# Performance work log

Hardware: AMD Instinct MI355X
Metric: run time of the kernel (lower is better)

Reference implementation:

```python
import jax, jax.numpy as jnp
import numpy as np

STRIPE = 8
EPS = 1e-5  # PyTorch BatchNorm default eps


def setup_inputs() -> dict:
    key = jax.random.key(0)
    ks = jax.random.split(key, 8)
    b, c, t, h, w = 4, 256, 8, 128, 64
    ic = c // 2  # inter_channels default = in_channels // 2
    scale = 0.02
    return {
        "x": jax.random.normal(ks[0], (b, c, t, h, w), jnp.float32),
        # 1x1 Conv3d weights are just channel-mixing matrices (out, in)
        "g_w": jax.random.normal(ks[1], (ic, c), jnp.float32) * scale,
        "g_b": jnp.zeros((ic,), jnp.float32),
        "theta_w": jax.random.normal(ks[2], (ic, c), jnp.float32) * scale,
        "theta_b": jnp.zeros((ic,), jnp.float32),
        "phi_w": jax.random.normal(ks[3], (ic, c), jnp.float32) * scale,
        "phi_b": jnp.zeros((ic,), jnp.float32),
        "W_w": jax.random.normal(ks[4], (c, ic), jnp.float32) * scale,
        "W_b": jnp.zeros((c,), jnp.float32),
        # BatchNorm3d (eval mode): original inits gamma=beta=0; use nonzero
        # gamma here so the reference output is non-trivial.
        "bn_gamma": jax.random.normal(ks[5], (c,), jnp.float32) * 0.1,
        "bn_beta": jax.random.normal(ks[6], (c,), jnp.float32) * 0.1,
        "bn_mean": jnp.zeros((c,), jnp.float32),
        "bn_var": jnp.ones((c,), jnp.float32),
    }


def reference(x, g_w, g_b, theta_w, theta_b, phi_w, phi_b,
              W_w, W_b, bn_gamma, bn_beta, bn_mean, bn_var):
    b, c, t, h, w = x.shape
    hs = h // STRIPE
    # stripe mean-pool: AdaptiveAvgPool2d(1) over each (hs, w) stripe region
    xr = x.reshape(b, c, t, STRIPE, hs, w)
    d = xr.mean(axis=(4, 5))                      # (b, c, t, stripe)
    S = t * STRIPE
    dn = d.reshape(b, c, S)                       # tokens: (b, c, S)
    # 1x1 conv3d projections == channel matmuls
    g = jnp.einsum('bcs,ic->bsi', dn, g_w) + g_b          # (b, S, ic)
    th = jnp.einsum('bcs,ic->bsi', dn, theta_w) + theta_b  # (b, S, ic)
    ph = jnp.einsum('bcs,ic->bsi', dn, phi_w) + phi_b      # (b, S, ic)
    # small self-attention over stripe tokens
    f = jnp.einsum('bsi,bri->bsr', th, ph)                 # (b, S, S)
    attn = jax.nn.softmax(f, axis=-1)                      # instance='soft'
    y = jnp.einsum('bsr,bri->bsi', attn, g)                # (b, S, ic)
    # output 1x1 conv + BatchNorm3d (eval mode, running stats)
    Wy = jnp.einsum('bsi,ci->bcs', y, W_w) + W_b[None, :, None]  # (b, c, S)
    inv = bn_gamma / jnp.sqrt(bn_var + EPS)
    Wy = (Wy - bn_mean[None, :, None]) * inv[None, :, None] + bn_beta[None, :, None]
    # broadcast each stripe value back over its (hs, w) region + residual
    Wy = Wy.reshape(b, c, t, STRIPE, 1, 1)
    z = (xr + Wy).reshape(b, c, t, h, w)
    return z
```

## Files before the change

### kernel.cpp

```cpp
#include <hip/hip_runtime.h>
#include <hip/hip_bf16.h>
#include <math.h>

#define B 4
#define C 256
#define T 8
#define H 128
#define WW 64
#define IC 128
#define S 64
#define NSTRIPE 8
#define HS 16
#define REGION 1024
#define EPS 1e-5f

__global__ void pool_kernel(const float* __restrict__ x, float* __restrict__ dn) {
    int sb = blockIdx.x;
    const float4* xr = (const float4*)(x + (size_t)sb * REGION);
    float4 v = xr[threadIdx.x];
    float sum = v.x + v.y + v.z + v.w;
    #pragma unroll
    for (int off = 32; off > 0; off >>= 1)
        sum += __shfl_down(sum, off, 64);
    __shared__ float ws[4];
    int wid = threadIdx.x >> 6;
    int lane = threadIdx.x & 63;
    if (lane == 0) ws[wid] = sum;
    __syncthreads();
    if (threadIdx.x == 0) {
        float tot = ws[0] + ws[1] + ws[2] + ws[3];
        dn[sb] = tot * (1.0f / (float)REGION);
    }
}

__global__ void proj_kernel(const float* __restrict__ dn,
                            const float* __restrict__ gw, const float* __restrict__ gb,
                            const float* __restrict__ tw, const float* __restrict__ tb,
                            const float* __restrict__ pw, const float* __restrict__ pb,
                            float* __restrict__ g, float* __restrict__ th,
                            float* __restrict__ ph) {
    int blk = blockIdx.x;
    int b = blk >> 6, s = blk & 63;
    __shared__ float dloc[C];
    for (int ch = threadIdx.x; ch < C; ch += blockDim.x)
        dloc[ch] = dn[(b * C + ch) * S + s];
    __syncthreads();
    int i = threadIdx.x;
    float ag = gb[i], at = tb[i], ap = pb[i];
    const float* gwr = gw + i * C;
    const float* twr = tw + i * C;
    const float* pwr = pw + i * C;
    for (int ch = 0; ch < C; ++ch) {
        float d = dloc[ch];
        ag = fmaf(d, gwr[ch], ag);
        at = fmaf(d, twr[ch], at);
        ap = fmaf(d, pwr[ch], ap);
    }
    size_t o = ((size_t)(b * S + s)) * IC + i;
    g[o] = ag; th[o] = at; ph[o] = ap;
}

__global__ void attn_kernel(const float* __restrict__ g,
                            const float* __restrict__ th,
                            const float* __restrict__ ph,
                            float* __restrict__ y) {
    int blk = blockIdx.x;
    int b = blk >> 6, s = blk & 63;
    __shared__ float p[S];
    __shared__ float thloc[IC];
    int tid = threadIdx.x;
    thloc[tid] = th[((size_t)(b * S + s)) * IC + tid];
    __syncthreads();
    if (tid < 64) {
        int r = tid;
        const float* phr = ph + ((size_t)(b * S + r)) * IC;
        float f = 0.0f;
        for (int i = 0; i < IC; ++i) f = fmaf(thloc[i], phr[i], f);
        float m = f;
        #pragma unroll
        for (int off = 32; off > 0; off >>= 1)
            m = fmaxf(m, __shfl_xor(m, off, 64));
        float e = __expf(f - m);
        float sum = e;
        #pragma unroll
        for (int off = 32; off > 0; off >>= 1)
            sum += __shfl_xor(sum, off, 64);
        p[r] = e / sum;
    }
    __syncthreads();
    int i = tid;
    float acc = 0.0f;
    for (int r = 0; r < S; ++r)
        acc = fmaf(p[r], g[((size_t)(b * S + r)) * IC + i], acc);
    y[((size_t)(b * S + s)) * IC + i] = acc;
}

__global__ void outproj_kernel(const float* __restrict__ y,
                               const float* __restrict__ Ww, const float* __restrict__ Wb,
                               const float* __restrict__ gamma, const float* __restrict__ beta,
                               const float* __restrict__ mean, const float* __restrict__ var,
                               float* __restrict__ wy) {
    int idx = blockIdx.x * blockDim.x + threadIdx.x;
    int s = idx & 63;
    int ch = (idx >> 6) & 255;
    int b = idx >> 14;
    const float* yr = y + ((size_t)(b * S + s)) * IC;
    const float* wr = Ww + (size_t)ch * IC;
    float acc = Wb[ch];
    for (int i = 0; i < IC; ++i) acc = fmaf(yr[i], wr[i], acc);
    float inv = gamma[ch] * rsqrtf(var[ch] + EPS);
    wy[idx] = (acc - mean[ch]) * inv + beta[ch];
}

__global__ void add_kernel(const float* __restrict__ x,
                           const float* __restrict__ wy,
                           float* __restrict__ out) {
    size_t f = (size_t)blockIdx.x * blockDim.x + threadIdx.x;
    const float4* x4 = (const float4*)x;
    float4* o4 = (float4*)out;
    float4 v = x4[f];
    float a = wy[f >> 8];
    v.x += a; v.y += a; v.z += a; v.w += a;
    o4[f] = v;
}

extern "C" void kernel_launch(void* const* d_in, const int* in_sizes, int n_in,
                              void* d_out, int out_size, void* d_ws, size_t ws_size,
                              hipStream_t stream) {
    const float* x       = (const float*)d_in[0];
    const float* g_w     = (const float*)d_in[1];
    const float* g_b     = (const float*)d_in[2];
    const float* theta_w = (const float*)d_in[3];
    const float* theta_b = (const float*)d_in[4];
    const float* phi_w   = (const float*)d_in[5];
    const float* phi_b   = (const float*)d_in[6];
    const float* W_w     = (const float*)d_in[7];
    const float* W_b     = (const float*)d_in[8];
    const float* bn_g    = (const float*)d_in[9];
    const float* bn_b    = (const float*)d_in[10];
    const float* bn_m    = (const float*)d_in[11];
    const float* bn_v    = (const float*)d_in[12];
    float* out = (float*)d_out;

    float* ws = (float*)d_ws;
    float* dn = ws;
    float* g  = dn + B * C * S;
    float* th = g  + B * S * IC;
    float* ph = th + B * S * IC;
    float* y  = ph + B * S * IC;
    float* wy = y  + B * S * IC;

    const int nRegions = B * C * T * NSTRIPE;
    pool_kernel<<<nRegions, 256, 0, stream>>>(x, dn);

    proj_kernel<<<B * S, IC, 0, stream>>>(dn, g_w, g_b, theta_w, theta_b,
                                          phi_w, phi_b, g, th, ph);

    attn_kernel<<<B * S, IC, 0, stream>>>(g, th, ph, y);

    outproj_kernel<<<(B * C * S) / 256, 256, 0, stream>>>(y, W_w, W_b,
                                                          bn_g, bn_b, bn_m, bn_v, wy);

    const size_t nVec4 = (size_t)B * C * T * H * WW / 4;
    add_kernel<<<(int)(nVec4 / 256), 256, 0, stream>>>(x, wy, out);
}
```

Baseline: 514.8 us.

## Fuse attention with output projection and retile pooling and projection kernels

Pooling now has one wavefront per region and writes the token-major layout (b,s,c), so the projection kernel can load its input with contiguous float4 reads. The projection kernel runs the three projections on 384 threads, one weight matrix per group of 128, using vectorized weight reads. Attention, the output 1x1 conv and BatchNorm are fused into one kernel that stages g in shared memory, which removes the y buffer and one launch. The add kernel reads the wy buffer with the new transposed indexing. The total time is still dominated by the memory-bound pool and add passes over x.

```diff
diff --git a/kernel.cpp b/kernel.cpp
--- a/kernel.cpp
+++ b/kernel.cpp
@@ -1,5 +1,4 @@
 #include <hip/hip_runtime.h>
-#include <hip/hip_bf16.h>
 #include <math.h>
 
 #define B 4
@@ -15,21 +14,24 @@
 #define EPS 1e-5f
 
 __global__ void pool_kernel(const float* __restrict__ x, float* __restrict__ dn) {
-    int sb = blockIdx.x;
+    int wid = threadIdx.x >> 6;
+    int lane = threadIdx.x & 63;
+    int sb = blockIdx.x * 4 + wid;
     const float4* xr = (const float4*)(x + (size_t)sb * REGION);
-    float4 v = xr[threadIdx.x];
-    float sum = v.x + v.y + v.z + v.w;
+    float sum = 0.0f;
+    #pragma unroll
+    for (int k = 0; k < 4; ++k) {
+        float4 v = xr[k * 64 + lane];
+        sum += v.x + v.y + v.z + v.w;
+    }
     #pragma unroll
     for (int off = 32; off > 0; off >>= 1)
         sum += __shfl_down(sum, off, 64);
-    __shared__ float ws[4];
-    int wid = threadIdx.x >> 6;
-    int lane = threadIdx.x & 63;
-    if (lane == 0) ws[wid] = sum;
-    __syncthreads();
-    if (threadIdx.x == 0) {
-        float tot = ws[0] + ws[1] + ws[2] + ws[3];
-        dn[sb] = tot * (1.0f / (float)REGION);
+    if (lane == 0) {
+        int b = sb >> 14;
+        int c = (sb >> 6) & 255;
+        int s = sb & 63;
+        dn[(((size_t)b << 6) | s) * C + c] = sum * (1.0f / (float)REGION);
     }
 }
 
@@ -40,76 +42,124 @@
                             float* __restrict__ g, float* __restrict__ th,
                             float* __restrict__ ph) {
     int blk = blockIdx.x;
-    int b = blk >> 6, s = blk & 63;
-    __shared__ float dloc[C];
-    for (int ch = threadIdx.x; ch < C; ch += blockDim.x)
-        dloc[ch] = dn[(b * C + ch) * S + s];
-    __syncthreads();
-    int i = threadIdx.x;
-    float ag = gb[i], at = tb[i], ap = pb[i];
-    const float* gwr = gw + i * C;
-    const float* twr = tw + i * C;
-    const float* pwr = pw + i * C;
-    for (int ch = 0; ch < C; ++ch) {
-        float d = dloc[ch];
-        ag = fmaf(d, gwr[ch], ag);
-        at = fmaf(d, twr[ch], at);
-        ap = fmaf(d, pwr[ch], ap);
-    }
-    size_t o = ((size_t)(b * S + s)) * IC + i;
-    g[o] = ag; th[o] = at; ph[o] = ap;
-}
-
-__global__ void attn_kernel(const float* __restrict__ g,
-                            const float* __restrict__ th,
-                            const float* __restrict__ ph,
-                            float* __restrict__ y) {
+    __shared__ float4 dloc[C / 4];
+    int tid = threadIdx.x;
+    if (tid < C / 4)
+        dloc[tid] = ((const float4*)(dn + (size_t)blk * C))[tid];
+    __syncthreads();
+    int p = tid >> 7;
+    int i = tid & 127;
+    const float* wsel = (p == 0) ? gw : (p == 1) ? tw : pw;
+    const float* bsel = (p == 0) ? gb : (p == 1) ? tb : pb;
+    float* osel      = (p == 0) ? g  : (p == 1) ? th : ph;
+    const float4* wr = (const float4*)(wsel + (size_t)i * C);
+    float4 a = {0.f, 0.f, 0.f, 0.f};
+    #pragma unroll 8
+    for (int k = 0; k < C / 4; ++k) {
+        float4 wv = wr[k];
+        float4 dv = dloc[k];
+        a.x = fmaf(dv.x, wv.x, a.x);
+        a.y = fmaf(dv.y, wv.y, a.y);
+        a.z = fmaf(dv.z, wv.z, a.z);
+        a.w = fmaf(dv.w, wv.w, a.w);
+    }
+    osel[(size_t)blk * IC + i] = a.x + a.y + a.z + a.w + bsel[i];
+}
+
+__global__ void attn_out_kernel(const float* __restrict__ g,
+                                const float* __restrict__ th,
+                                const float* __restrict__ ph,
+                                const float* __restrict__ Ww, const float* __restrict__ Wb,
+                                const float* __restrict__ gamma, const float* __restrict__ beta,
+                                const float* __restrict__ mean, const float* __restrict__ var,
+                                float* __restrict__ wy) {
     int blk = blockIdx.x;
-    int b = blk >> 6, s = blk & 63;
-    __shared__ float p[S];
+    int b = blk >> 6;
+    int tid = threadIdx.x;
+
     __shared__ float thloc[IC];
-    int tid = threadIdx.x;
-    thloc[tid] = th[((size_t)(b * S + s)) * IC + tid];
-    __syncthreads();
+    __shared__ float gloc[S][IC];
+    __shared__ float sc[S];
+    __shared__ float pvals[S];
+    __shared__ float ypart[2][IC];
+    __shared__ float yloc[IC];
+
+    if (tid < IC) thloc[tid] = th[(size_t)blk * IC + tid];
+    {
+        const float4* gsrc = (const float4*)(g + (size_t)(b * S) * IC);
+        float4* gdst = (float4*)&gloc[0][0];
+        #pragma unroll
+        for (int k = 0; k < (S * IC / 4) / 256; ++k)
+            gdst[k * 256 + tid] = gsrc[k * 256 + tid];
+    }
+    __syncthreads();
+
+    {
+        int r = tid >> 2, q = tid & 3;
+        const float4* phr = (const float4*)(ph + (size_t)(b * S + r) * IC) + q * 8;
+        const float4* th4 = (const float4*)thloc + q * 8;
+        float4 a = {0.f, 0.f, 0.f, 0.f};
+        #pragma unroll
+        for (int k = 0; k < 8; ++k) {
+            float4 pv = phr[k];
+            float4 tv = th4[k];
+            a.x = fmaf(tv.x, pv.x, a.x);
+            a.y = fmaf(tv.y, pv.y, a.y);
+            a.z = fmaf(tv.z, pv.z, a.z);
+            a.w = fmaf(tv.w, pv.w, a.w);
+        }
+        float f = a.x + a.y + a.z + a.w;
+        f += __shfl_xor(f, 1, 64);
+        f += __shfl_xor(f, 2, 64);
+        if (q == 0) sc[r] = f;
+    }
+    __syncthreads();
+
     if (tid < 64) {
-        int r = tid;
-        const float* phr = ph + ((size_t)(b * S + r)) * IC;
-        float f = 0.0f;
-        for (int i = 0; i < IC; ++i) f = fmaf(thloc[i], phr[i], f);
-        float m = f;
+        float v = sc[tid];
+        float m = v;
         #pragma unroll
         for (int off = 32; off > 0; off >>= 1)
             m = fmaxf(m, __shfl_xor(m, off, 64));
-        float e = __expf(f - m);
+        float e = __expf(v - m);
         float sum = e;
         #pragma unroll
         for (int off = 32; off > 0; off >>= 1)
             sum += __shfl_xor(sum, off, 64);
-        p[r] = e / sum;
-    }
-    __syncthreads();
-    int i = tid;
-    float acc = 0.0f;
-    for (int r = 0; r < S; ++r)
-        acc = fmaf(p[r], g[((size_t)(b * S + r)) * IC + i], acc);
-    y[((size_t)(b * S + s)) * IC + i] = acc;
-}
-
-__global__ void outproj_kernel(const float* __restrict__ y,
-                               const float* __restrict__ Ww, const float* __restrict__ Wb,
-                               const float* __restrict__ gamma, const float* __restrict__ beta,
-                               const float* __restrict__ mean, const float* __restrict__ var,
-                               float* __restrict__ wy) {
-    int idx = blockIdx.x * blockDim.x + threadIdx.x;
-    int s = idx & 63;
-    int ch = (idx >> 6) & 255;
-    int b = idx >> 14;
-    const float* yr = y + ((size_t)(b * S + s)) * IC;
-    const float* wr = Ww + (size_t)ch * IC;
-    float acc = Wb[ch];
-    for (int i = 0; i < IC; ++i) acc = fmaf(yr[i], wr[i], acc);
-    float inv = gamma[ch] * rsqrtf(var[ch] + EPS);
-    wy[idx] = (acc - mean[ch]) * inv + beta[ch];
+        pvals[tid] = e / sum;
+    }
+    __syncthreads();
+
+    {
+        int i = tid & 127, half = tid >> 7;
+        float acc = 0.0f;
+        int r0 = half * 32;
+        #pragma unroll 8
+        for (int r = r0; r < r0 + 32; ++r)
+            acc = fmaf(pvals[r], gloc[r][i], acc);
+        ypart[half][i] = acc;
+    }
+    __syncthreads();
+    if (tid < IC) yloc[tid] = ypart[0][tid] + ypart[1][tid];
+    __syncthreads();
+
+    {
+        const float4* wr = (const float4*)(Ww + (size_t)tid * IC);
+        const float4* y4 = (const float4*)yloc;
+        float4 o = {0.f, 0.f, 0.f, 0.f};
+        #pragma unroll 8
+        for (int k = 0; k < IC / 4; ++k) {
+            float4 wv = wr[k];
+            float4 yv = y4[k];
+            o.x = fmaf(yv.x, wv.x, o.x);
+            o.y = fmaf(yv.y, wv.y, o.y);
+            o.z = fmaf(yv.z, wv.z, o.z);
+            o.w = fmaf(yv.w, wv.w, o.w);
+        }
+        float acc = o.x + o.y + o.z + o.w + Wb[tid];
+        float inv = gamma[tid] * rsqrtf(var[tid] + EPS);
+        wy[(size_t)blk * C + tid] = (acc - mean[tid]) * inv + beta[tid];
+    }
 }
 
 __global__ void add_kernel(const float* __restrict__ x,
@@ -119,7 +169,11 @@
     const float4* x4 = (const float4*)x;
     float4* o4 = (float4*)out;
     float4 v = x4[f];
-    float a = wy[f >> 8];
+    size_t rgn = f >> 8;
+    int b = (int)(rgn >> 14);
+    int c = (int)(rgn >> 6) & 255;
+    int s = (int)rgn & 63;
+    float a = wy[((((size_t)b << 6) | s) << 8) | c];
     v.x += a; v.y += a; v.z += a; v.w += a;
     o4[f] = v;
 }
@@ -147,19 +201,16 @@
     float* g  = dn + B * C * S;
     float* th = g  + B * S * IC;
     float* ph = th + B * S * IC;
-    float* y  = ph + B * S * IC;
-    float* wy = y  + B * S * IC;
+    float* wy = ph + B * S * IC;
 
     const int nRegions = B * C * T * NSTRIPE;
-    pool_kernel<<<nRegions, 256, 0, stream>>>(x, dn);
-
-    proj_kernel<<<B * S, IC, 0, stream>>>(dn, g_w, g_b, theta_w, theta_b,
-                                          phi_w, phi_b, g, th, ph);
-
-    attn_kernel<<<B * S, IC, 0, stream>>>(g, th, ph, y);
-
-    outproj_kernel<<<(B * C * S) / 256, 256, 0, stream>>>(y, W_w, W_b,
-                                                          bn_g, bn_b, bn_m, bn_v, wy);
+    pool_kernel<<<nRegions / 4, 256, 0, stream>>>(x, dn);
+
+    proj_kernel<<<B * S, 384, 0, stream>>>(dn, g_w, g_b, theta_w, theta_b,
+                                           phi_w, phi_b, g, th, ph);
+
+    attn_out_kernel<<<B * S, 256, 0, stream>>>(g, th, ph, W_w, W_b,
+                                               bn_g, bn_b, bn_m, bn_v, wy);
 
     const size_t nVec4 = (size_t)B * C * T * H * WW / 4;
     add_kernel<<<(int)(nVec4 / 256), 256, 0, stream>>>(x, wy, out);
```

New measurement: 514.2 us. Within noise of the previous version (-0.1%).
